# Optimization experiments

Measured on AMD Instinct MI355X. Metric: run time of the kernel, lower is better.

## Reference

```python
import jax, jax.numpy as jnp
import numpy as np

DIM = 1024
NUM_HEADS = 16
HEAD_DIM = DIM // NUM_HEADS
B, T = 2, 2048


def _rope_tables(seq_len, head_dim, dtype=jnp.float32):
    inv_freq = 1.0 / (10000.0 ** (jnp.arange(0, head_dim, 2, dtype=jnp.float32) / head_dim))
    t = jnp.arange(seq_len, dtype=jnp.float32)
    freqs = jnp.einsum('i,j->ij', t, inv_freq)            # [T, head_dim/2]
    emb = jnp.concatenate((freqs, freqs), axis=-1)         # [T, head_dim]
    return jnp.cos(emb).astype(dtype), jnp.sin(emb).astype(dtype)


def _rotate_half(x):
    x1, x2 = x[..., : x.shape[-1] // 2], x[..., x.shape[-1] // 2 :]
    return jnp.concatenate((-x2, x1), axis=-1)


def setup_inputs() -> dict:
    key = jax.random.key(0)
    ks = jax.random.split(key, 5)
    s = 1.0 / np.sqrt(DIM)
    return {
        'x': jax.random.normal(ks[0], (B, T, DIM), dtype=jnp.float32),
        'w_q': jax.random.normal(ks[1], (DIM, DIM), dtype=jnp.float32) * s,
        'w_k': jax.random.normal(ks[2], (DIM, DIM), dtype=jnp.float32) * s,
        'w_v': jax.random.normal(ks[3], (DIM, DIM), dtype=jnp.float32) * s,
        'w_out': jax.random.normal(ks[4], (DIM, DIM), dtype=jnp.float32) * s,
    }


def reference(x, w_q, w_k, w_v, w_out):
    Bn, Tn, C = x.shape
    scale = HEAD_DIM ** -0.5
    # nn.Linear(bias=False): y = x @ W^T; reshape to [B, H, T, Dh]
    def proj(w):
        y = jnp.einsum('btc,dc->btd', x, w)
        return y.reshape(Bn, Tn, NUM_HEADS, HEAD_DIM).transpose(0, 2, 1, 3)
    q, k, v = proj(w_q), proj(w_k), proj(w_v)
    cos, sin = _rope_tables(Tn, HEAD_DIM, x.dtype)         # [T, Dh], broadcasts over B,H
    q = q * cos + _rotate_half(q) * sin
    k = k * cos + _rotate_half(k) * sin
    attn = jnp.einsum('bhqd,bhkd->bhqk', q, k) * scale     # [B,H,T,T]
    attn = jax.nn.softmax(attn, axis=-1)
    out = jnp.einsum('bhqk,bhkd->bhqd', attn, v)           # [B,H,T,Dh]
    out = out.transpose(0, 2, 1, 3).reshape(Bn, Tn, C)
    return jnp.einsum('btc,dc->btd', out, w_out)
```

## Files before the change

kernel.cpp:

```cpp
#include <hip/hip_runtime.h>


typedef _Float16 f16;
typedef f16 f16x8 __attribute__((ext_vector_type(8)));
typedef __fp16 fp16x2 __attribute__((ext_vector_type(2)));
typedef float f32x4 __attribute__((ext_vector_type(4)));
typedef float f32x16 __attribute__((ext_vector_type(16)));
typedef unsigned int u32;
typedef unsigned short u16;

union V16 { uint4 u; f16x8 h; };

__device__ __forceinline__ float exp2_fast(float x) {
#if __has_builtin(__builtin_amdgcn_exp2f)
  return __builtin_amdgcn_exp2f(x);
#else
  return __expf(x * 0.69314718056f);
#endif
}

__device__ __forceinline__ u32 pkrtz(float a, float b) {
  union { fp16x2 h; u32 u; } cv;
  cv.h = __builtin_amdgcn_cvt_pkrtz(a, b);
  return cv.u;
}

#define PLSWAP(a, b)                                                          \
  asm volatile("s_nop 1\n\tv_permlane32_swap_b32 %0, %1" : "+v"(a), "+v"(b))

#define GLDS(src, dst) __builtin_amdgcn_global_load_lds(                      \
    (const __attribute__((address_space(1))) void*)(const void*)(src),        \
    (__attribute__((address_space(3))) void*)(void*)(dst), 16, 0, 0)

#define WAITBAR(N) do {                                                       \
    asm volatile("s_waitcnt vmcnt(" #N ")" ::: "memory");                     \
    __builtin_amdgcn_s_barrier();                                             \
    __builtin_amdgcn_sched_barrier(0);                                        \
  } while (0)

__global__ __launch_bounds__(256) void rope_tables_kernel(float* __restrict__ cosT,
                                                          float* __restrict__ sinT) {
  int i = blockIdx.x * 256 + threadIdx.x;
  int t = i >> 5, j = i & 31;
  float inv = 1.0f / powf(10000.0f, (float)(2 * j) * (1.0f / 64.0f));
  float ang = (float)t * inv;
  double a = (double)ang;
  cosT[i] = (float)cos(a);
  sinT[i] = (float)sin(a);
}

__global__ __launch_bounds__(256)
void cvt5_kernel(const float* __restrict__ x,  const float* __restrict__ wq,
                 const float* __restrict__ wk, const float* __restrict__ wv,
                 const float* __restrict__ wo,
                 f16* __restrict__ xh, f16* __restrict__ W3,
                 f16* __restrict__ woh) {
  int bx = blockIdx.x;
  const float* src; f16* dst; int i;
  if (bx < 4096) {
    src = x; dst = xh; i = bx * 256 + threadIdx.x;
  } else {
    int b = (bx - 4096) >> 10;
    i = ((bx - 4096) & 1023) * 256 + threadIdx.x;
    src = (b == 0) ? wq : (b == 1) ? wk : (b == 2) ? wv : wo;
    dst = (b == 3) ? woh : W3 + (size_t)b * 1048576;
  }
  float4 v = ((const float4*)src)[i];
  union { f16 h[4]; uint2 u; } cv;
  cv.h[0] = (f16)v.x; cv.h[1] = (f16)v.y; cv.h[2] = (f16)v.z; cv.h[3] = (f16)v.w;
  ((uint2*)dst)[i] = cv.u;
}

__global__ __launch_bounds__(256)
void gemm_qkv_kernel(const f16* __restrict__ X,
                     const f16* __restrict__ W3,
                     f16* __restrict__ Qo, f16* __restrict__ Ko,
                     f16* __restrict__ VTo,
                     const float* __restrict__ cosT,
                     const float* __restrict__ sinT) {
  __shared__ u16 lds[3][8192];

  const int tid = threadIdx.x, lane = tid & 63, w = tid >> 6;
  const int wr = w >> 1, wc = w & 1;
  const int c = lane & 15, g = lane >> 4;
  const int m0 = blockIdx.x * 128;
  const int by = blockIdx.y;
  const int wsel = by >> 3, hp = by & 7, h0 = hp * 2;
  const f16* Wb = W3 + (size_t)wsel * (1024 * 1024) + (size_t)hp * 128 * 1024;

  const int n1 = tid, n2 = tid + 256;
  const int r1 = n1 >> 2, gc1 = (n1 & 3) ^ ((n1 >> 3) & 3);
  const int r2 = n2 >> 2, gc2 = (n2 & 3) ^ ((n2 >> 3) & 3);
  const f16* gA1 = X + (size_t)(m0 + r1) * 1024 + gc1 * 8;
  const f16* gA2 = X + (size_t)(m0 + r2) * 1024 + gc2 * 8;
  const f16* gB1 = Wb + (size_t)r1 * 1024 + gc1 * 8;
  const f16* gB2 = Wb + (size_t)r2 * 1024 + gc2 * 8;
  const int dA1 = n1 * 8, dA2 = n2 * 8;
  const int dB1 = 4096 + n1 * 8, dB2 = 4096 + n2 * 8;

  f32x4 acc[4][4];
  const f32x4 zero = {0.f, 0.f, 0.f, 0.f};
#pragma unroll
  for (int mi = 0; mi < 4; ++mi)
#pragma unroll
    for (int ni = 0; ni < 4; ++ni) acc[mi][ni] = zero;

#define STAGE_QKV(buf, kt) do {                                               \
    const int ko = (kt) * 32;                                                 \
    GLDS(gA1 + ko, &lds[buf][dA1]);                                           \
    GLDS(gA2 + ko, &lds[buf][dA2]);                                           \
    GLDS(gB1 + ko, &lds[buf][dB1]);                                           \
    GLDS(gB2 + ko, &lds[buf][dB2]);                                           \
  } while (0)

  const int swz = (g ^ ((c >> 1) & 3)) * 8;

  STAGE_QKV(0, 0);
  STAGE_QKV(1, 1);
  WAITBAR(4);

  int cur = 0, nx2 = 2;
  for (int kt = 0; kt < 32; ++kt) {
    if (kt < 30) STAGE_QKV(nx2, kt + 2);
    V16 a[4], b[4];
#pragma unroll
    for (int mi = 0; mi < 4; ++mi)
      a[mi].u = *(const uint4*)&lds[cur][(wr * 64 + mi * 16 + c) * 32 + swz];
#pragma unroll
    for (int ni = 0; ni < 4; ++ni)
      b[ni].u = *(const uint4*)&lds[cur][4096 + (wc * 64 + ni * 16 + c) * 32 + swz];
    __builtin_amdgcn_s_setprio(1);
#pragma unroll
    for (int mi = 0; mi < 4; ++mi)
#pragma unroll
      for (int ni = 0; ni < 4; ++ni)
        acc[mi][ni] = __builtin_amdgcn_mfma_f32_16x16x32_f16(a[mi].h, b[ni].h, acc[mi][ni], 0, 0, 0);
    __builtin_amdgcn_s_setprio(0);
    if (kt < 30) WAITBAR(4); else WAITBAR(0);
    cur = (cur == 2) ? 0 : cur + 1;
    nx2 = (nx2 == 2) ? 0 : nx2 + 1;
  }

  if (wsel < 2) {
    f16* Out = (wsel == 0) ? Qo : Ko;
    const float psc = (wsel == 0) ? 0.18033688f : 1.0f;
    const int head = h0 + wc;
#pragma unroll
    for (int mi = 0; mi < 4; ++mi)
#pragma unroll
      for (int r = 0; r < 4; ++r) {
        int m = m0 + wr * 64 + mi * 16 + g * 4 + r;
        int bb = m >> 11, t = m & 2047;
        float co0 = cosT[t * 32 + c],      si0 = sinT[t * 32 + c];
        float co1 = cosT[t * 32 + 16 + c], si1 = sinT[t * 32 + 16 + c];
#pragma unroll
        for (int ni = 0; ni < 4; ++ni) {
          int d = ni * 16 + c;
          float co = (ni & 1) ? co1 : co0;
          float si = (ni & 1) ? si1 : si0;
          float partner = acc[mi][ni ^ 2][r];
          float v = (acc[mi][ni][r] * co + ((d < 32) ? -partner : partner) * si) * psc;
          Out[((size_t)(bb * 16 + head) * 2048 + t) * 64 + d] = (f16)v;
        }
      }
  } else {
    u16* sT = &lds[0][0];
    const int head = h0 + wc;
    const int bbv = m0 >> 11;
    const int t0 = (m0 & 2047) + wr * 64;
#pragma unroll
    for (int mi = 0; mi < 4; ++mi)
#pragma unroll
      for (int ni = 0; ni < 4; ++ni)
#pragma unroll
        for (int r = 0; r < 4; ++r) {
          int dl = ni * 16 + c;
          int tl = mi * 16 + g * 4 + r;
          union { f16 h; u16 u; } cv; cv.h = (f16)acc[mi][ni][r];
          sT[w * 4608 + dl * 72 + tl] = cv.u;
        }
    f16* dst = VTo + ((size_t)(bbv * 16 + head) * 64 + lane) * 2048 + t0;
    const u16* srcp = &sT[w * 4608 + lane * 72];
#pragma unroll
    for (int s = 0; s < 16; ++s)
      *(uint2*)(dst + s * 4) = *(const uint2*)(srcp + s * 4);
  }
}

__global__ __launch_bounds__(256)
void gemm_out_kernel(const f16* __restrict__ AH, const f16* __restrict__ BH,
                     float* __restrict__ outF) {
  __shared__ u16 lds[3][8192];

  const int tid = threadIdx.x, lane = tid & 63, w = tid >> 6;
  const int wr = w >> 1, wc = w & 1;
  const int c = lane & 15, g = lane >> 4;
  const int m0 = blockIdx.x * 128, n0 = blockIdx.y * 128;

  const int n1 = tid, n2 = tid + 256;
  const int r1 = n1 >> 2, gc1 = (n1 & 3) ^ ((n1 >> 3) & 3);
  const int r2 = n2 >> 2, gc2 = (n2 & 3) ^ ((n2 >> 3) & 3);
  const f16* gA1 = AH + (size_t)(m0 + r1) * 1024 + gc1 * 8;
  const f16* gA2 = AH + (size_t)(m0 + r2) * 1024 + gc2 * 8;
  const f16* gB1 = BH + (size_t)(n0 + r1) * 1024 + gc1 * 8;
  const f16* gB2 = BH + (size_t)(n0 + r2) * 1024 + gc2 * 8;
  const int dA1 = n1 * 8, dA2 = n2 * 8;
  const int dB1 = 4096 + n1 * 8, dB2 = 4096 + n2 * 8;

  f32x4 acc[4][4];
  const f32x4 zero = {0.f, 0.f, 0.f, 0.f};
#pragma unroll
  for (int mi = 0; mi < 4; ++mi)
#pragma unroll
    for (int ni = 0; ni < 4; ++ni) acc[mi][ni] = zero;

#define STAGE_OUT(buf, kt) do {                                               \
    const int ko = (kt) * 32;                                                 \
    GLDS(gA1 + ko, &lds[buf][dA1]);                                           \
    GLDS(gA2 + ko, &lds[buf][dA2]);                                           \
    GLDS(gB1 + ko, &lds[buf][dB1]);                                           \
    GLDS(gB2 + ko, &lds[buf][dB2]);                                           \
  } while (0)

  const int swz = (g ^ ((c >> 1) & 3)) * 8;

  STAGE_OUT(0, 0);
  STAGE_OUT(1, 1);
  WAITBAR(4);

  int cur = 0, nx2 = 2;
  for (int kt = 0; kt < 32; ++kt) {
    if (kt < 30) STAGE_OUT(nx2, kt + 2);
    V16 a[4], b[4];
#pragma unroll
    for (int mi = 0; mi < 4; ++mi)
      a[mi].u = *(const uint4*)&lds[cur][(wr * 64 + mi * 16 + c) * 32 + swz];
#pragma unroll
    for (int ni = 0; ni < 4; ++ni)
      b[ni].u = *(const uint4*)&lds[cur][4096 + (wc * 64 + ni * 16 + c) * 32 + swz];
    __builtin_amdgcn_s_setprio(1);
#pragma unroll
    for (int mi = 0; mi < 4; ++mi)
#pragma unroll
      for (int ni = 0; ni < 4; ++ni)
        acc[mi][ni] = __builtin_amdgcn_mfma_f32_16x16x32_f16(a[mi].h, b[ni].h, acc[mi][ni], 0, 0, 0);
    __builtin_amdgcn_s_setprio(0);
    if (kt < 30) WAITBAR(4); else WAITBAR(0);
    cur = (cur == 2) ? 0 : cur + 1;
    nx2 = (nx2 == 2) ? 0 : nx2 + 1;
  }

#pragma unroll
  for (int mi = 0; mi < 4; ++mi)
#pragma unroll
    for (int r = 0; r < 4; ++r) {
      int m = m0 + wr * 64 + mi * 16 + g * 4 + r;
#pragma unroll
      for (int ni = 0; ni < 4; ++ni)
        outF[(size_t)m * 1024 + n0 + wc * 64 + ni * 16 + c] = acc[mi][ni][r];
    }
}

__global__ __launch_bounds__(256, 2)
void attn_kernel(const f16* __restrict__ Q, const f16* __restrict__ K,
                 const f16* __restrict__ VT, f16* __restrict__ OH) {
  __shared__ u16 sKV[3][8192];
  __shared__ u16 sT16[4][32][36];

  const int tid = threadIdx.x, lane = tid & 63, wid = tid >> 6;
  const int q32 = lane & 31, hi = lane >> 5;
  const int bx = blockIdx.x;
  const int bh = (bx & 7) + 8 * (bx >> 7);
  const int qt = (bx >> 3) & 15;
  const int bb = bh >> 4, hh = bh & 15;
  const int q0 = qt * 128 + wid * 32;

  V16 qf[4];
  const f16* qp = Q + ((size_t)bh * 2048 + q0 + q32) * 64 + 8 * hi;
#pragma unroll
  for (int kd = 0; kd < 4; ++kd)
    qf[kd].u = *(const uint4*)(qp + 16 * kd);

  f32x16 o0 = 0.0f, o1 = 0.0f;
  float lsum = 0.f;

  const int srow = tid >> 3, scol = tid & 7;
  const f16* gK = K  + ((size_t)bh * 2048 + srow) * 64 + scol * 8;
  const f16* gV = VT + ((size_t)bh * 64 + srow) * 2048 + scol * 8;
  const int dst0 = srow * 128 + ((scol ^ (srow & 7)) << 4);
  const int dst1 = dst0 + 32 * 128;

  uint4 rk0, rk1, rv0, rv1;
#define LOADT(kt) do {                                                        \
    const f16* pk = gK + (size_t)(kt) * 4096;                                 \
    rk0 = *(const uint4*)(pk);                                                \
    rk1 = *(const uint4*)(pk + 32 * 64);                                      \
    const f16* pv = gV + (size_t)(kt) * 64;                                   \
    rv0 = *(const uint4*)(pv);                                                \
    rv1 = *(const uint4*)(pv + 32 * 2048);                                    \
  } while (0)
#define WRITET(buf) do {                                                      \
    char* base_ = (char*)&sKV[buf][0];                                        \
    *(uint4*)(base_ + dst0) = rk0; *(uint4*)(base_ + dst1) = rk1;             \
    *(uint4*)(base_ + 8192 + dst0) = rv0; *(uint4*)(base_ + 8192 + dst1) = rv1;\
  } while (0)

  const int swzrow = (q32 & 7) << 4;

#define QKT(D0, D1, buf) do {                                                 \
    D0 = 0.0f; D1 = 0.0f;                                                     \
    const char* kb_ = (const char*)&sKV[buf][0];                              \
    __builtin_amdgcn_s_setprio(1);                                            \
    _Pragma("unroll")                                                         \
    for (int kd = 0; kd < 4; ++kd) {                                          \
      const int off = ((32 * kd + 16 * hi) ^ swzrow);                         \
      V16 kf0, kf1;                                                           \
      kf0.u = *(const uint4*)(kb_ + q32 * 128 + off);                         \
      kf1.u = *(const uint4*)(kb_ + (32 + q32) * 128 + off);                  \
      D0 = __builtin_amdgcn_mfma_f32_32x32x16_f16(kf0.h, qf[kd].h, D0, 0, 0, 0);\
      D1 = __builtin_amdgcn_mfma_f32_32x32x16_f16(kf1.h, qf[kd].h, D1, 0, 0, 0);\
    }                                                                         \
    __builtin_amdgcn_s_setprio(0);                                            \
  } while (0)

#define SOFTMAX_PB() do {                                                     \
    u32 c0[8], c1[8];                                                         \
    _Pragma("unroll")                                                         \
    for (int m = 0; m < 8; ++m) {                                             \
      float p0 = exp2_fast(st0[2 * m]);                                       \
      float p1 = exp2_fast(st0[2 * m + 1]);                                   \
      lsum += p0 + p1; c0[m] = pkrtz(p0, p1);                                 \
      float p2 = exp2_fast(st1[2 * m]);                                       \
      float p3 = exp2_fast(st1[2 * m + 1]);                                   \
      lsum += p2 + p3; c1[m] = pkrtz(p2, p3);                                 \
    }                                                                         \
    { u32 y0 = c0[0], x0 = c0[2]; PLSWAP(y0, x0);                             \
      u32 y1 = c0[1], x1 = c0[3]; PLSWAP(y1, x1);                             \
      pB[0].u.x = y0; pB[0].u.y = y1; pB[0].u.z = x0; pB[0].u.w = x1;         \
      u32 y2 = c0[4], x2 = c0[6]; PLSWAP(y2, x2);                             \
      u32 y3 = c0[5], x3 = c0[7]; PLSWAP(y3, x3);                             \
      pB[1].u.x = y2; pB[1].u.y = y3; pB[1].u.z = x2; pB[1].u.w = x3;         \
      u32 y4 = c1[0], x4 = c1[2]; PLSWAP(y4, x4);                             \
      u32 y5 = c1[1], x5 = c1[3]; PLSWAP(y5, x5);                             \
      pB[2].u.x = y4; pB[2].u.y = y5; pB[2].u.z = x4; pB[2].u.w = x5;         \
      u32 y6 = c1[4], x6 = c1[6]; PLSWAP(y6, x6);                             \
      u32 y7 = c1[5], x7 = c1[7]; PLSWAP(y7, x7);                             \
      pB[3].u.x = y6; pB[3].u.y = y7; pB[3].u.z = x6; pB[3].u.w = x7; }       \
  } while (0)

#define PVOP(buf) do {                                                        \
    const char* vb_ = (const char*)&sKV[buf][0] + 8192;                       \
    __builtin_amdgcn_s_setprio(1);                                            \
    _Pragma("unroll")                                                         \
    for (int ks = 0; ks < 4; ++ks) {                                          \
      const int off = ((32 * ks + 16 * hi) ^ swzrow);                         \
      V16 vf0, vf1;                                                           \
      vf0.u = *(const uint4*)(vb_ + q32 * 128 + off);                         \
      vf1.u = *(const uint4*)(vb_ + (32 + q32) * 128 + off);                  \
      o0 = __builtin_amdgcn_mfma_f32_32x32x16_f16(vf0.h, pB[ks].h, o0, 0, 0, 0);\
      o1 = __builtin_amdgcn_mfma_f32_32x32x16_f16(vf1.h, pB[ks].h, o1, 0, 0, 0);\
    }                                                                         \
    __builtin_amdgcn_s_setprio(0);                                            \
  } while (0)

  LOADT(0);
  WRITET(0);
  __syncthreads();
  LOADT(1);
  f32x16 st0, st1;
  QKT(st0, st1, 0);

  V16 pB[4];
  int bw = 1, bp = 0;
  for (int kt = 0; kt < 31; ++kt) {
    WRITET(bw);
    __syncthreads();
    if (kt < 30) LOADT(kt + 2);
    SOFTMAX_PB();
    QKT(st0, st1, bw);
    PVOP(bp);
    bp = bw; bw = (bw == 2) ? 0 : bw + 1;
  }
  SOFTMAX_PB();
  PVOP(bp);

  const float l_run = lsum + __shfl_xor(lsum, 32, 64);
  const float inv = 1.0f / l_run;
  const int qr = lane >> 1, dh = (lane & 1) * 16;
#pragma unroll
  for (int dt = 0; dt < 2; ++dt) {
#pragma unroll
    for (int r = 0; r < 16; ++r) {
      float v = (dt ? o1[r] : o0[r]) * inv;
      union { f16 h; u16 u; } cv; cv.h = (f16)v;
      sT16[wid][q32][(r & 3) + 8 * (r >> 2) + 4 * hi] = cv.u;
    }
    __syncthreads();
    const u16* sp = &sT16[wid][qr][dh];
    uint2 a0 = *(const uint2*)(sp + 0),  a1 = *(const uint2*)(sp + 4);
    uint2 a2 = *(const uint2*)(sp + 8),  a3 = *(const uint2*)(sp + 12);
    size_t gbase = ((size_t)bb * 2048 + q0 + qr) * 1024 + hh * 64 + 32 * dt + dh;
    *(uint2*)(OH + gbase + 0)  = a0;
    *(uint2*)(OH + gbase + 4)  = a1;
    *(uint2*)(OH + gbase + 8)  = a2;
    *(uint2*)(OH + gbase + 12) = a3;
    __syncthreads();
  }
}

extern "C" void kernel_launch(void* const* d_in, const int* in_sizes, int n_in,
                              void* d_out, int out_size, void* d_ws, size_t ws_size,
                              hipStream_t stream) {
  const float* x  = (const float*)d_in[0];
  const float* wq = (const float*)d_in[1];
  const float* wk = (const float*)d_in[2];
  const float* wv = (const float*)d_in[3];
  const float* wo = (const float*)d_in[4];

  constexpr size_t SZ_X   = 4096ull * 1024 * 2;
  constexpr size_t SZ_W   = 1024ull * 1024 * 2;
  constexpr size_t SZ_QKV = 2ull * 16 * 2048 * 64 * 2;
  constexpr size_t SZ_TBL = 2048ull * 32 * 4;
  constexpr size_t NEED = SZ_X + 4 * SZ_W + 3 * SZ_QKV + 2 * SZ_TBL;
  if (ws_size < NEED) return;

  char* ws = (char*)d_ws;
  f16* xh  = (f16*)(ws);
  f16* W3  = (f16*)(ws + SZ_X);
  f16* woh = (f16*)(ws + SZ_X + 3 * SZ_W);
  char* p  = ws + SZ_X + 4 * SZ_W;
  f16* qb  = (f16*)(p);            p += SZ_QKV;
  f16* kb  = (f16*)(p);            p += SZ_QKV;
  f16* vT  = (f16*)(p);            p += SZ_QKV;
  float* cosT = (float*)(p);       p += SZ_TBL;
  float* sinT = (float*)(p);
  f16* oh = xh;

  rope_tables_kernel<<<256, 256, 0, stream>>>(cosT, sinT);
  cvt5_kernel<<<8192, 256, 0, stream>>>(x, wq, wk, wv, wo, xh, W3, woh);

  gemm_qkv_kernel<<<dim3(32, 24), 256, 0, stream>>>(xh, W3, qb, kb, vT,
                                                    cosT, sinT);

  attn_kernel<<<512, 256, 0, stream>>>(qb, kb, vT, oh);

  gemm_out_kernel<<<dim3(32, 8), 256, 0, stream>>>(oh, woh, (float*)d_out);
}
```

Baseline: 120.1 us.

## Split attention KV range across two blocks and merge partial outputs

Reworks the attention kernel so each wave handles 64 query rows (two 32-row groups) and each block covers only half of the key/value sequence, so every K/V tile staged in shared memory feeds twice as many MFMAs. Unnormalized partial outputs and row sums go to workspace, and a new merge kernel adds the two halves and normalizes. K/V staging moves to direct global-to-LDS loads with a 4-deep buffer ring. The merge step adds an extra kernel launch and an extra round trip through global memory, and partial results are stored in fp16 before normalization. This relies on the softmax having no running max, which the code already assumes.

```diff
diff --git a/kernel.cpp b/kernel.cpp
--- a/kernel.cpp
+++ b/kernel.cpp
@@ -263,53 +263,51 @@
 
 __global__ __launch_bounds__(256, 2)
 void attn_kernel(const f16* __restrict__ Q, const f16* __restrict__ K,
-                 const f16* __restrict__ VT, f16* __restrict__ OH) {
-  __shared__ u16 sKV[3][8192];
+                 const f16* __restrict__ VT,
+                 f16* __restrict__ OP, float* __restrict__ LP) {
+  __shared__ u16 sKV[4][8192];
   __shared__ u16 sT16[4][32][36];
 
   const int tid = threadIdx.x, lane = tid & 63, wid = tid >> 6;
   const int q32 = lane & 31, hi = lane >> 5;
   const int bx = blockIdx.x;
   const int bh = (bx & 7) + 8 * (bx >> 7);
-  const int qt = (bx >> 3) & 15;
-  const int bb = bh >> 4, hh = bh & 15;
-  const int q0 = qt * 128 + wid * 32;
-
-  V16 qf[4];
-  const f16* qp = Q + ((size_t)bh * 2048 + q0 + q32) * 64 + 8 * hi;
-#pragma unroll
-  for (int kd = 0; kd < 4; ++kd)
-    qf[kd].u = *(const uint4*)(qp + 16 * kd);
-
-  f32x16 o0 = 0.0f, o1 = 0.0f;
-  float lsum = 0.f;
-
-  const int srow = tid >> 3, scol = tid & 7;
-  const f16* gK = K  + ((size_t)bh * 2048 + srow) * 64 + scol * 8;
-  const f16* gV = VT + ((size_t)bh * 64 + srow) * 2048 + scol * 8;
-  const int dst0 = srow * 128 + ((scol ^ (srow & 7)) << 4);
-  const int dst1 = dst0 + 32 * 128;
-
-  uint4 rk0, rk1, rv0, rv1;
-#define LOADT(kt) do {                                                        \
-    const f16* pk = gK + (size_t)(kt) * 4096;                                 \
-    rk0 = *(const uint4*)(pk);                                                \
-    rk1 = *(const uint4*)(pk + 32 * 64);                                      \
-    const f16* pv = gV + (size_t)(kt) * 64;                                   \
-    rv0 = *(const uint4*)(pv);                                                \
-    rv1 = *(const uint4*)(pv + 32 * 2048);                                    \
-  } while (0)
-#define WRITET(buf) do {                                                      \
-    char* base_ = (char*)&sKV[buf][0];                                        \
-    *(uint4*)(base_ + dst0) = rk0; *(uint4*)(base_ + dst1) = rk1;             \
-    *(uint4*)(base_ + 8192 + dst0) = rv0; *(uint4*)(base_ + 8192 + dst1) = rv1;\
+  const int rest = (bx >> 3) & 15;
+  const int qt = rest & 7, half = rest >> 3;
+  const int qbase = qt * 256 + wid * 64;
+  const int t0 = half * 16;
+
+  V16 qfa[4], qfb[4];
+  const f16* qpa = Q + ((size_t)bh * 2048 + qbase + q32) * 64 + 8 * hi;
+#pragma unroll
+  for (int kd = 0; kd < 4; ++kd) {
+    qfa[kd].u = *(const uint4*)(qpa + 16 * kd);
+    qfb[kd].u = *(const uint4*)(qpa + 32 * 64 + 16 * kd);
+  }
+
+  f32x16 oa0 = 0.0f, oa1 = 0.0f, ob0 = 0.0f, ob1 = 0.0f;
+  f32x16 sa0, sa1, sb0, sb1;
+  float lsa = 0.f, lsb = 0.f;
+
+  const int rr = tid >> 3;
+  const int sc = ((tid & 7) ^ (rr & 7)) * 8;
+  const f16* gK1 = K + ((size_t)bh * 2048 + t0 * 64 + rr) * 64 + sc;
+  const f16* gK2 = gK1 + 32 * 64;
+  const f16* gV1 = VT + ((size_t)bh * 64 + rr) * 2048 + t0 * 64 + sc;
+  const f16* gV2 = gV1 + 32 * 2048;
+
+#define STAGE_A(buf, j) do {                                                  \
+    GLDS(gK1 + (j) * 4096, &sKV[buf][tid * 8]);                               \
+    GLDS(gK2 + (j) * 4096, &sKV[buf][2048 + tid * 8]);                        \
+    GLDS(gV1 + (j) * 64,   &sKV[buf][4096 + tid * 8]);                        \
+    GLDS(gV2 + (j) * 64,   &sKV[buf][6144 + tid * 8]);                        \
   } while (0)
 
   const int swzrow = (q32 & 7) << 4;
 
-#define QKT(D0, D1, buf) do {                                                 \
-    D0 = 0.0f; D1 = 0.0f;                                                     \
-    const char* kb_ = (const char*)&sKV[buf][0];                              \
+#define QKT2(BUF) do {                                                        \
+    sa0 = 0.0f; sa1 = 0.0f; sb0 = 0.0f; sb1 = 0.0f;                           \
+    const char* kb_ = (const char*)&sKV[BUF][0];                              \
     __builtin_amdgcn_s_setprio(1);                                            \
     _Pragma("unroll")                                                         \
     for (int kd = 0; kd < 4; ++kd) {                                          \
@@ -317,39 +315,41 @@
       V16 kf0, kf1;                                                           \
       kf0.u = *(const uint4*)(kb_ + q32 * 128 + off);                         \
       kf1.u = *(const uint4*)(kb_ + (32 + q32) * 128 + off);                  \
-      D0 = __builtin_amdgcn_mfma_f32_32x32x16_f16(kf0.h, qf[kd].h, D0, 0, 0, 0);\
-      D1 = __builtin_amdgcn_mfma_f32_32x32x16_f16(kf1.h, qf[kd].h, D1, 0, 0, 0);\
+      sa0 = __builtin_amdgcn_mfma_f32_32x32x16_f16(kf0.h, qfa[kd].h, sa0, 0, 0, 0);\
+      sa1 = __builtin_amdgcn_mfma_f32_32x32x16_f16(kf1.h, qfa[kd].h, sa1, 0, 0, 0);\
+      sb0 = __builtin_amdgcn_mfma_f32_32x32x16_f16(kf0.h, qfb[kd].h, sb0, 0, 0, 0);\
+      sb1 = __builtin_amdgcn_mfma_f32_32x32x16_f16(kf1.h, qfb[kd].h, sb1, 0, 0, 0);\
     }                                                                         \
     __builtin_amdgcn_s_setprio(0);                                            \
   } while (0)
 
-#define SOFTMAX_PB() do {                                                     \
+#define SMAX(S0, S1, PB, LS) do {                                             \
     u32 c0[8], c1[8];                                                         \
     _Pragma("unroll")                                                         \
     for (int m = 0; m < 8; ++m) {                                             \
-      float p0 = exp2_fast(st0[2 * m]);                                       \
-      float p1 = exp2_fast(st0[2 * m + 1]);                                   \
-      lsum += p0 + p1; c0[m] = pkrtz(p0, p1);                                 \
-      float p2 = exp2_fast(st1[2 * m]);                                       \
-      float p3 = exp2_fast(st1[2 * m + 1]);                                   \
-      lsum += p2 + p3; c1[m] = pkrtz(p2, p3);                                 \
+      float p0 = exp2_fast(S0[2 * m]);                                        \
+      float p1 = exp2_fast(S0[2 * m + 1]);                                    \
+      LS += p0 + p1; c0[m] = pkrtz(p0, p1);                                   \
+      float p2 = exp2_fast(S1[2 * m]);                                        \
+      float p3 = exp2_fast(S1[2 * m + 1]);                                    \
+      LS += p2 + p3; c1[m] = pkrtz(p2, p3);                                   \
     }                                                                         \
     { u32 y0 = c0[0], x0 = c0[2]; PLSWAP(y0, x0);                             \
       u32 y1 = c0[1], x1 = c0[3]; PLSWAP(y1, x1);                             \
-      pB[0].u.x = y0; pB[0].u.y = y1; pB[0].u.z = x0; pB[0].u.w = x1;         \
+      PB[0].u.x = y0; PB[0].u.y = y1; PB[0].u.z = x0; PB[0].u.w = x1;         \
       u32 y2 = c0[4], x2 = c0[6]; PLSWAP(y2, x2);                             \
       u32 y3 = c0[5], x3 = c0[7]; PLSWAP(y3, x3);                             \
-      pB[1].u.x = y2; pB[1].u.y = y3; pB[1].u.z = x2; pB[1].u.w = x3;         \
+      PB[1].u.x = y2; PB[1].u.y = y3; PB[1].u.z = x2; PB[1].u.w = x3;         \
       u32 y4 = c1[0], x4 = c1[2]; PLSWAP(y4, x4);                             \
       u32 y5 = c1[1], x5 = c1[3]; PLSWAP(y5, x5);                             \
-      pB[2].u.x = y4; pB[2].u.y = y5; pB[2].u.z = x4; pB[2].u.w = x5;         \
+      PB[2].u.x = y4; PB[2].u.y = y5; PB[2].u.z = x4; PB[2].u.w = x5;         \
       u32 y6 = c1[4], x6 = c1[6]; PLSWAP(y6, x6);                             \
       u32 y7 = c1[5], x7 = c1[7]; PLSWAP(y7, x7);                             \
-      pB[3].u.x = y6; pB[3].u.y = y7; pB[3].u.z = x6; pB[3].u.w = x7; }       \
-  } while (0)
-
-#define PVOP(buf) do {                                                        \
-    const char* vb_ = (const char*)&sKV[buf][0] + 8192;                       \
+      PB[3].u.x = y6; PB[3].u.y = y7; PB[3].u.z = x6; PB[3].u.w = x7; }       \
+  } while (0)
+
+#define PV2(BUF) do {                                                         \
+    const char* vb_ = (const char*)&sKV[BUF][0] + 8192;                       \
     __builtin_amdgcn_s_setprio(1);                                            \
     _Pragma("unroll")                                                         \
     for (int ks = 0; ks < 4; ++ks) {                                          \
@@ -357,55 +357,79 @@
       V16 vf0, vf1;                                                           \
       vf0.u = *(const uint4*)(vb_ + q32 * 128 + off);                         \
       vf1.u = *(const uint4*)(vb_ + (32 + q32) * 128 + off);                  \
-      o0 = __builtin_amdgcn_mfma_f32_32x32x16_f16(vf0.h, pB[ks].h, o0, 0, 0, 0);\
-      o1 = __builtin_amdgcn_mfma_f32_32x32x16_f16(vf1.h, pB[ks].h, o1, 0, 0, 0);\
+      oa0 = __builtin_amdgcn_mfma_f32_32x32x16_f16(vf0.h, pBa[ks].h, oa0, 0, 0, 0);\
+      oa1 = __builtin_amdgcn_mfma_f32_32x32x16_f16(vf1.h, pBa[ks].h, oa1, 0, 0, 0);\
+      ob0 = __builtin_amdgcn_mfma_f32_32x32x16_f16(vf0.h, pBb[ks].h, ob0, 0, 0, 0);\
+      ob1 = __builtin_amdgcn_mfma_f32_32x32x16_f16(vf1.h, pBb[ks].h, ob1, 0, 0, 0);\
     }                                                                         \
     __builtin_amdgcn_s_setprio(0);                                            \
   } while (0)
 
-  LOADT(0);
-  WRITET(0);
-  __syncthreads();
-  LOADT(1);
-  f32x16 st0, st1;
-  QKT(st0, st1, 0);
-
-  V16 pB[4];
-  int bw = 1, bp = 0;
-  for (int kt = 0; kt < 31; ++kt) {
-    WRITET(bw);
-    __syncthreads();
-    if (kt < 30) LOADT(kt + 2);
-    SOFTMAX_PB();
-    QKT(st0, st1, bw);
-    PVOP(bp);
-    bp = bw; bw = (bw == 2) ? 0 : bw + 1;
-  }
-  SOFTMAX_PB();
-  PVOP(bp);
-
-  const float l_run = lsum + __shfl_xor(lsum, 32, 64);
-  const float inv = 1.0f / l_run;
+  V16 pBa[4], pBb[4];
+
+  STAGE_A(0, 0);
+  STAGE_A(1, 1);
+  WAITBAR(4);
+  QKT2(0);
+
+  for (int kt = 0; kt < 16; ++kt) {
+    if (kt < 14) STAGE_A((kt + 2) & 3, kt + 2);
+    SMAX(sa0, sa1, pBa, lsa);
+    SMAX(sb0, sb1, pBb, lsb);
+    if (kt < 14) { WAITBAR(4); } else { WAITBAR(0); }
+    if (kt < 15) QKT2((kt + 1) & 3);
+    PV2(kt & 3);
+  }
+
+  lsa += __shfl_xor(lsa, 32, 64);
+  lsb += __shfl_xor(lsb, 32, 64);
+  const size_t lbase = (size_t)(half * 32 + bh) * 2048 + qbase;
+  if (hi == 0) {
+    LP[lbase + q32] = lsa;
+    LP[lbase + 32 + q32] = lsb;
+  }
+
   const int qr = lane >> 1, dh = (lane & 1) * 16;
 #pragma unroll
-  for (int dt = 0; dt < 2; ++dt) {
-#pragma unroll
-    for (int r = 0; r < 16; ++r) {
-      float v = (dt ? o1[r] : o0[r]) * inv;
-      union { f16 h; u16 u; } cv; cv.h = (f16)v;
-      sT16[wid][q32][(r & 3) + 8 * (r >> 2) + 4 * hi] = cv.u;
+  for (int grp = 0; grp < 2; ++grp) {
+#pragma unroll
+    for (int dt = 0; dt < 2; ++dt) {
+#pragma unroll
+      for (int r = 0; r < 16; ++r) {
+        float v = grp ? (dt ? ob1[r] : ob0[r]) : (dt ? oa1[r] : oa0[r]);
+        union { f16 h; u16 u; } cv; cv.h = (f16)v;
+        sT16[wid][q32][(r & 3) + 8 * (r >> 2) + 4 * hi] = cv.u;
+      }
+      __syncthreads();
+      const u16* sp = &sT16[wid][qr][dh];
+      uint2 a0 = *(const uint2*)(sp + 0),  a1 = *(const uint2*)(sp + 4);
+      uint2 a2 = *(const uint2*)(sp + 8),  a3 = *(const uint2*)(sp + 12);
+      size_t gbase = ((size_t)(half * 32 + bh) * 2048 + qbase + grp * 32 + qr) * 64
+                     + 32 * dt + dh;
+      *(uint2*)(OP + gbase + 0)  = a0;
+      *(uint2*)(OP + gbase + 4)  = a1;
+      *(uint2*)(OP + gbase + 8)  = a2;
+      *(uint2*)(OP + gbase + 12) = a3;
+      __syncthreads();
     }
-    __syncthreads();
-    const u16* sp = &sT16[wid][qr][dh];
-    uint2 a0 = *(const uint2*)(sp + 0),  a1 = *(const uint2*)(sp + 4);
-    uint2 a2 = *(const uint2*)(sp + 8),  a3 = *(const uint2*)(sp + 12);
-    size_t gbase = ((size_t)bb * 2048 + q0 + qr) * 1024 + hh * 64 + 32 * dt + dh;
-    *(uint2*)(OH + gbase + 0)  = a0;
-    *(uint2*)(OH + gbase + 4)  = a1;
-    *(uint2*)(OH + gbase + 8)  = a2;
-    *(uint2*)(OH + gbase + 12) = a3;
-    __syncthreads();
-  }
+  }
+}
+
+__global__ __launch_bounds__(256)
+void merge_kernel(const f16* __restrict__ OP, const float* __restrict__ LP,
+                  f16* __restrict__ OH) {
+  int i = blockIdx.x * 256 + threadIdx.x;
+  int d8 = i & 7, q = (i >> 3) & 2047, bh = i >> 14;
+  size_t pa = ((size_t)bh * 2048 + q) * 64 + d8 * 8;
+  size_t pb = pa + (size_t)32 * 2048 * 64;
+  union { uint4 u; f16x8 h; } va, vb, vr;
+  va.u = *(const uint4*)(OP + pa);
+  vb.u = *(const uint4*)(OP + pb);
+  float inv = 1.0f / (LP[bh * 2048 + q] + LP[65536 + bh * 2048 + q]);
+  f16 s = (f16)inv;
+  vr.h = (va.h + vb.h) * s;
+  int bb = bh >> 4, hh = bh & 15;
+  *(uint4*)(OH + ((size_t)bb * 2048 + q) * 1024 + hh * 64 + d8 * 8) = vr.u;
 }
 
 extern "C" void kernel_launch(void* const* d_in, const int* in_sizes, int n_in,
@@ -421,7 +445,9 @@
   constexpr size_t SZ_W   = 1024ull * 1024 * 2;
   constexpr size_t SZ_QKV = 2ull * 16 * 2048 * 64 * 2;
   constexpr size_t SZ_TBL = 2048ull * 32 * 4;
-  constexpr size_t NEED = SZ_X + 4 * SZ_W + 3 * SZ_QKV + 2 * SZ_TBL;
+  constexpr size_t SZ_OP  = 2ull * 32 * 2048 * 64 * 2;
+  constexpr size_t SZ_LP  = 2ull * 32 * 2048 * 4;
+  constexpr size_t NEED = SZ_X + 4 * SZ_W + 3 * SZ_QKV + 2 * SZ_TBL + SZ_OP + SZ_LP;
   if (ws_size < NEED) return;
 
   char* ws = (char*)d_ws;
@@ -433,7 +459,9 @@
   f16* kb  = (f16*)(p);            p += SZ_QKV;
   f16* vT  = (f16*)(p);            p += SZ_QKV;
   float* cosT = (float*)(p);       p += SZ_TBL;
-  float* sinT = (float*)(p);
+  float* sinT = (float*)(p);       p += SZ_TBL;
+  f16* OPart = (f16*)(p);          p += SZ_OP;
+  float* LPart = (float*)(p);
   f16* oh = xh;
 
   rope_tables_kernel<<<256, 256, 0, stream>>>(cosT, sinT);
@@ -442,7 +470,8 @@
   gemm_qkv_kernel<<<dim3(32, 24), 256, 0, stream>>>(xh, W3, qb, kb, vT,
                                                     cosT, sinT);
 
-  attn_kernel<<<512, 256, 0, stream>>>(qb, kb, vT, oh);
+  attn_kernel<<<512, 256, 0, stream>>>(qb, kb, vT, OPart, LPart);
+  merge_kernel<<<2048, 256, 0, stream>>>(OPart, LPart, oh);
 
   gemm_out_kernel<<<dim3(32, 8), 256, 0, stream>>>(oh, woh, (float*)d_out);
 }
```

After: 123.1 us. 2.5% more time.
